# Performance work log

Hardware: AMD Instinct MI355X
Metric: run time of the kernel (lower is better)

Reference implementation:

```python
import jax, jax.numpy as jnp
import numpy as np

N_NODES = 50000
N_EDGES = 500000
N_GRAPHS = 256
D_IN, D_H1, D_H2, D_H3, D_OUT = 768, 256, 128, 64, 2


def _glorot(key, shape):
    fan_in, fan_out = shape[1], shape[0]
    lim = float(np.sqrt(6.0 / (fan_in + fan_out)))
    return jax.random.uniform(key, shape, jnp.float32, -lim, lim)


def setup_inputs() -> dict:
    key = jax.random.key(0)
    ks = jax.random.split(key, 12)
    x = jax.random.normal(ks[0], (N_NODES, D_IN), jnp.float32)
    edge_index = jax.random.randint(ks[1], (2, N_EDGES), 0, N_NODES, jnp.int64)
    batch = jnp.sort(jax.random.randint(ks[2], (N_NODES,), 0, N_GRAPHS, jnp.int64))
    return {
        "x": x,
        "edge_index": edge_index,
        "batch": batch,
        # SAGEConv1: out = lin_l(mean_aggr) + lin_r(x); bias only on lin_l (PyG default)
        "W1_l": _glorot(ks[3], (D_H1, D_IN)),
        "b1_l": jnp.zeros((D_H1,), jnp.float32),
        "W1_r": _glorot(ks[4], (D_H1, D_IN)),
        # SAGEConv2
        "W2_l": _glorot(ks[5], (D_H2, D_H1)),
        "b2_l": jnp.zeros((D_H2,), jnp.float32),
        "W2_r": _glorot(ks[6], (D_H2, D_H1)),
        # MLP head
        "W3": _glorot(ks[7], (D_H3, D_H2)),
        "b3": jnp.zeros((D_H3,), jnp.float32),
        "W4": _glorot(ks[8], (D_OUT, D_H3)),
        "b4": jnp.zeros((D_OUT,), jnp.float32),
    }


def _sage_conv(x, src, dst, deg_inv, W_l, b_l, W_r):
    # mean aggregation of neighbor features: scatter-add then divide by in-degree
    aggr = jax.ops.segment_sum(x[src], dst, num_segments=N_NODES)  # [N, d]
    aggr = aggr * deg_inv[:, None]
    return aggr @ W_l.T + b_l + x @ W_r.T


def reference(x, edge_index, batch, W1_l, b1_l, W1_r, W2_l, b2_l, W2_r, W3, b3, W4, b4):
    src, dst = edge_index[0], edge_index[1]
    deg = jax.ops.segment_sum(jnp.ones((N_EDGES,), x.dtype), dst, num_segments=N_NODES)
    deg_inv = jnp.where(deg > 0, 1.0 / jnp.maximum(deg, 1.0), 0.0)

    h = jax.nn.relu(_sage_conv(x, src, dst, deg_inv, W1_l, b1_l, W1_r))
    h = jax.nn.relu(_sage_conv(h, src, dst, deg_inv, W2_l, b2_l, W2_r))

    # global_mean_pool over graph ids
    pooled = jax.ops.segment_sum(h, batch, num_segments=N_GRAPHS)  # [G, 128]
    cnt = jax.ops.segment_sum(jnp.ones((N_NODES,), h.dtype), batch, num_segments=N_GRAPHS)
    pooled = pooled / jnp.maximum(cnt, 1.0)[:, None]

    # dropout is identity in eval mode
    h = pooled @ W3.T + b3
    h = h @ W4.T + b4
    return jax.nn.softmax(h, axis=-1)
```

## Files before the change

### kernel.cpp

```cpp
#include <hip/hip_runtime.h>
#include <cstdint>
#include <cstddef>

#define N_NODES 50000
#define N_EDGES 500000
#define N_GRAPHS 256
#define D_IN 768
#define D_H1 256
#define D_H2 128

typedef __attribute__((ext_vector_type(8))) __bf16 bf16x8;
typedef __attribute__((ext_vector_type(4))) float f32x4;

__device__ __forceinline__ float bf2f(uint32_t u) {
    union { uint32_t i; float f; } v; v.i = u << 16; return v.f;
}
__device__ __forceinline__ uint32_t f2bf(float f) {
    union { float f; uint32_t i; } v; v.f = f;
    uint32_t u = v.i;
    return (u + 0x7FFFu + ((u >> 16) & 1u)) >> 16;
}

__device__ __forceinline__ void pack_chunk(const float* __restrict__ p,
                                           uint16_t* __restrict__ out, int c) {
    float4 u = *(const float4*)p, v = *(const float4*)(p + 4);
    uint4 o;
    o.x = f2bf(u.x) | (f2bf(u.y) << 16);
    o.y = f2bf(u.z) | (f2bf(u.w) << 16);
    o.z = f2bf(v.x) | (f2bf(v.y) << 16);
    o.w = f2bf(v.z) | (f2bf(v.w) << 16);
    *(uint4*)(out + (size_t)c * 8) = o;
}

#define PACKA_BLKS 18750
#define PACKW1_BLKS 192
#define PACKW2_BLKS 32
#define HIST_BLKS 1954
__global__ __launch_bounds__(256) void k_pack_hist(
    const float* __restrict__ x, uint16_t* __restrict__ xp,
    const float* __restrict__ W1l, const float* __restrict__ W1r, uint16_t* __restrict__ W1p,
    const float* __restrict__ W2l, const float* __restrict__ W2r, uint16_t* __restrict__ W2p,
    const int* __restrict__ e_dst, int* __restrict__ deg)
{
    int b = blockIdx.x;
    if (b < PACKA_BLKS) {
        int c = b * 256 + threadIdx.x;
        int l = c & 63, t = c >> 6;
        int kt = t % 24, mt = t / 24;
        int fr = l & 15, fq = l >> 4;
        pack_chunk(x + (size_t)(mt * 16 + fr) * 768 + kt * 32 + fq * 8, xp, c);
    } else if (b < PACKA_BLKS + PACKW1_BLKS) {
        int c = (b - PACKA_BLKS) * 256 + threadIdx.x;
        int l = c & 63, t = c >> 6;
        int kt = t % 24, mt = t / 24;
        int fr = l & 15, fq = l >> 4;
        int row = mt * 16 + fr;
        const float* src = (row < 256) ? (W1l + (size_t)row * 768)
                                       : (W1r + (size_t)(row - 256) * 768);
        pack_chunk(src + kt * 32 + fq * 8, W1p, c);
    } else if (b < PACKA_BLKS + PACKW1_BLKS + PACKW2_BLKS) {
        int c = (b - PACKA_BLKS - PACKW1_BLKS) * 256 + threadIdx.x;
        int l = c & 63, t = c >> 6;
        int kt = t % 8, mt = t / 8;
        int fr = l & 15, fq = l >> 4;
        int row = mt * 16 + fr;
        const float* src = (row < 128) ? (W2l + (size_t)row * 256)
                                       : (W2r + (size_t)(row - 128) * 256);
        pack_chunk(src + kt * 32 + fq * 8, W2p, c);
    } else {
        int e = (b - PACKA_BLKS - PACKW1_BLKS - PACKW2_BLKS) * 256 + threadIdx.x;
        if (e < N_EDGES) atomicAdd(&deg[e_dst[e]], 1);
    }
}

__global__ void k_scan1(const int* __restrict__ deg, int* __restrict__ row_ex,
                        int* __restrict__ bsum, int n) {
    __shared__ int buf[256];
    int t = threadIdx.x, i = blockIdx.x * 256 + t;
    int v = (i < n) ? deg[i] : 0;
    buf[t] = v; __syncthreads();
    for (int off = 1; off < 256; off <<= 1) {
        int u = (t >= off) ? buf[t - off] : 0;
        __syncthreads(); buf[t] += u; __syncthreads();
    }
    if (i < n) row_ex[i] = buf[t] - v;
    if (t == 255) bsum[blockIdx.x] = buf[255];
}
__global__ void k_scan23(const int* __restrict__ deg, const int* __restrict__ bsum,
                         int* __restrict__ row_start, float* __restrict__ deg_inv,
                         int n, int nb) {
    __shared__ int buf[256];
    int t = threadIdx.x;
    int v = (t < nb) ? bsum[t] : 0;
    buf[t] = v; __syncthreads();
    for (int off = 1; off < 256; off <<= 1) {
        int u = (t >= off) ? buf[t - off] : 0;
        __syncthreads(); buf[t] += u; __syncthreads();
    }
    int b = blockIdx.x;
    int boff = buf[b] - ((b < nb) ? bsum[b] : 0);
    int i = b * 256 + t;
    if (i < n) {
        row_start[i] += boff;
        int d = deg[i];
        deg_inv[i] = (d > 0) ? (1.0f / (float)d) : 0.0f;
    }
    if (b == 0 && t == 0) row_start[n] = N_EDGES;
}

#define G1_BLKS 784
__global__ __launch_bounds__(256, 2) void k_gemm1_fill(
    const uint16_t* __restrict__ Ap, const uint16_t* __restrict__ Bp,
    uint16_t* __restrict__ Cl, uint16_t* __restrict__ Cr,
    const int* __restrict__ e_src, const int* __restrict__ e_dst,
    const int* __restrict__ row_start, int* __restrict__ cursor,
    int* __restrict__ csr_src)
{
    if (blockIdx.x >= G1_BLKS) {
        int e = (blockIdx.x - G1_BLKS) * 256 + threadIdx.x;
        if (e < N_EDGES) {
            int d = e_dst[e];
            int pos = row_start[d] + atomicAdd(&cursor[d], 1);
            csr_src[pos] = e_src[e];
        }
        return;
    }
    const int i = blockIdx.x;
    const int pr = (i >> 4) * 8 + (i & 7);
    const int half = (i >> 3) & 1;
    if (pr >= 391) return;
    const int KT = 24, M = N_NODES;
    const int tid = threadIdx.x;
    const int wave = tid >> 6, lane = tid & 63;
    const int fr = lane & 15, fq = lane >> 4;
    const int bm = pr * 128;
    const int wm = (wave >> 1) * 64, wn = (wave & 1) * 128;
    const int mtiles = (M + 15) >> 4;

    const bf16x8* ap[4];
    const bf16x8* bp[8];
    #pragma unroll
    for (int mi = 0; mi < 4; ++mi) {
        int mt = ((bm + wm) >> 4) + mi;
        if (mt > mtiles - 1) mt = mtiles - 1;
        ap[mi] = (const bf16x8*)Ap + (size_t)mt * KT * 64 + lane;
    }
    #pragma unroll
    for (int ni = 0; ni < 8; ++ni) {
        int nt = ((half * 256 + wn) >> 4) + ni;
        bp[ni] = (const bf16x8*)Bp + (size_t)nt * KT * 64 + lane;
    }

    f32x4 acc[4][8] = {};
    bf16x8 a0[4], b0[8], a1[4], b1[8];

    auto lA = [&](int kt, bf16x8* d) {
        #pragma unroll
        for (int mi = 0; mi < 4; ++mi) d[mi] = ap[mi][kt * 64];
    };
    auto lB = [&](int kt, bf16x8* d) {
        #pragma unroll
        for (int ni = 0; ni < 8; ++ni) d[ni] = bp[ni][kt * 64];
    };
    auto step = [&](bf16x8* a, bf16x8* b) {
        #pragma unroll
        for (int mi = 0; mi < 4; ++mi)
            #pragma unroll
            for (int ni = 0; ni < 8; ++ni)
                acc[mi][ni] = __builtin_amdgcn_mfma_f32_16x16x32_bf16(
                    a[mi], b[ni], acc[mi][ni], 0, 0, 0);
    };

    lA(0, a0); lB(0, b0);
    for (int ks = 0; ks < KT; ks += 2) {
        lA(ks + 1, a1); lB(ks + 1, b1);
        step(a0, b0);
        if (ks + 2 < KT) { lA(ks + 2, a0); lB(ks + 2, b0); }
        step(a1, b1);
    }

    uint16_t* __restrict__ C = half ? Cr : Cl;
    #pragma unroll
    for (int mi = 0; mi < 4; ++mi) {
        #pragma unroll
        for (int r = 0; r < 4; ++r) {
            int row = bm + wm + mi * 16 + fq * 4 + r;
            if (row >= M) continue;
            #pragma unroll
            for (int ni = 0; ni < 8; ++ni) {
                int col = wn + ni * 16 + fr;
                C[(size_t)row * 256 + col] = (uint16_t)f2bf(acc[mi][ni][r]);
            }
        }
    }
}

__global__ __launch_bounds__(256, 2) void k_mgemm(
    const uint16_t* __restrict__ Ap, const uint16_t* __restrict__ Bp,
    uint16_t* __restrict__ C, int M, int N, int KT)
{
    const int tid = threadIdx.x;
    const int wave = tid >> 6, lane = tid & 63;
    const int fr = lane & 15, fq = lane >> 4;
    const int bn = blockIdx.x * 256, bm = blockIdx.y * 128;
    const int wm = (wave >> 1) * 64, wn = (wave & 1) * 128;
    const int mtiles = (M + 15) >> 4;

    const bf16x8* ap[4];
    const bf16x8* bp[8];
    #pragma unroll
    for (int mi = 0; mi < 4; ++mi) {
        int mt = ((bm + wm) >> 4) + mi;
        if (mt > mtiles - 1) mt = mtiles - 1;
        ap[mi] = (const bf16x8*)Ap + (size_t)mt * KT * 64 + lane;
    }
    #pragma unroll
    for (int ni = 0; ni < 8; ++ni) {
        int nt = ((bn + wn) >> 4) + ni;
        bp[ni] = (const bf16x8*)Bp + (size_t)nt * KT * 64 + lane;
    }

    f32x4 acc[4][8] = {};
    bf16x8 a0[4], b0[8], a1[4], b1[8];

    auto lA = [&](int kt, bf16x8* d) {
        #pragma unroll
        for (int mi = 0; mi < 4; ++mi) d[mi] = ap[mi][kt * 64];
    };
    auto lB = [&](int kt, bf16x8* d) {
        #pragma unroll
        for (int ni = 0; ni < 8; ++ni) d[ni] = bp[ni][kt * 64];
    };
    auto step = [&](bf16x8* a, bf16x8* b) {
        #pragma unroll
        for (int mi = 0; mi < 4; ++mi)
            #pragma unroll
            for (int ni = 0; ni < 8; ++ni)
                acc[mi][ni] = __builtin_amdgcn_mfma_f32_16x16x32_bf16(
                    a[mi], b[ni], acc[mi][ni], 0, 0, 0);
    };

    lA(0, a0); lB(0, b0);
    for (int ks = 0; ks < KT; ks += 2) {
        lA(ks + 1, a1); lB(ks + 1, b1);
        step(a0, b0);
        if (ks + 2 < KT) { lA(ks + 2, a0); lB(ks + 2, b0); }
        step(a1, b1);
    }

    #pragma unroll
    for (int mi = 0; mi < 4; ++mi) {
        #pragma unroll
        for (int r = 0; r < 4; ++r) {
            int row = bm + wm + mi * 16 + fq * 4 + r;
            if (row >= M) continue;
            #pragma unroll
            for (int ni = 0; ni < 8; ++ni) {
                int col = bn + wn + ni * 16 + fr;
                C[(size_t)row * N + col] = (uint16_t)f2bf(acc[mi][ni][r]);
            }
        }
    }
}

__global__ __launch_bounds__(256) void k_agg1(
    const uint16_t* __restrict__ yl, const uint16_t* __restrict__ yr,
    const int* __restrict__ row_start, const int* __restrict__ csr,
    const float* __restrict__ deg_inv, const float* __restrict__ bias,
    uint16_t* __restrict__ h1p)
{
    int node = blockIdx.x * 8 + (threadIdx.x >> 5);
    if (node >= N_NODES) return;
    int c = threadIdx.x & 31;
    int s = row_start[node], e = row_start[node + 1];
    float a[8] = {};
    int p = s;
    for (; p + 1 < e; p += 2) {
        uint4 t0 = *(const uint4*)(yl + (size_t)csr[p] * 256 + c * 8);
        uint4 t1 = *(const uint4*)(yl + (size_t)csr[p + 1] * 256 + c * 8);
        a[0] += bf2f(t0.x & 0xFFFF) + bf2f(t1.x & 0xFFFF);
        a[1] += bf2f(t0.x >> 16)    + bf2f(t1.x >> 16);
        a[2] += bf2f(t0.y & 0xFFFF) + bf2f(t1.y & 0xFFFF);
        a[3] += bf2f(t0.y >> 16)    + bf2f(t1.y >> 16);
        a[4] += bf2f(t0.z & 0xFFFF) + bf2f(t1.z & 0xFFFF);
        a[5] += bf2f(t0.z >> 16)    + bf2f(t1.z >> 16);
        a[6] += bf2f(t0.w & 0xFFFF) + bf2f(t1.w & 0xFFFF);
        a[7] += bf2f(t0.w >> 16)    + bf2f(t1.w >> 16);
    }
    if (p < e) {
        uint4 t0 = *(const uint4*)(yl + (size_t)csr[p] * 256 + c * 8);
        a[0] += bf2f(t0.x & 0xFFFF); a[1] += bf2f(t0.x >> 16);
        a[2] += bf2f(t0.y & 0xFFFF); a[3] += bf2f(t0.y >> 16);
        a[4] += bf2f(t0.z & 0xFFFF); a[5] += bf2f(t0.z >> 16);
        a[6] += bf2f(t0.w & 0xFFFF); a[7] += bf2f(t0.w >> 16);
    }
    float w = deg_inv[node];
    uint4 tx = *(const uint4*)(yr + (size_t)node * 256 + c * 8);
    float4 b0 = *(const float4*)(bias + c * 8);
    float4 b1 = *(const float4*)(bias + c * 8 + 4);
    float v0 = fmaxf(a[0] * w + bf2f(tx.x & 0xFFFF) + b0.x, 0.f);
    float v1 = fmaxf(a[1] * w + bf2f(tx.x >> 16)    + b0.y, 0.f);
    float v2 = fmaxf(a[2] * w + bf2f(tx.y & 0xFFFF) + b0.z, 0.f);
    float v3 = fmaxf(a[3] * w + bf2f(tx.y >> 16)    + b0.w, 0.f);
    float v4 = fmaxf(a[4] * w + bf2f(tx.z & 0xFFFF) + b1.x, 0.f);
    float v5 = fmaxf(a[5] * w + bf2f(tx.z >> 16)    + b1.y, 0.f);
    float v6 = fmaxf(a[6] * w + bf2f(tx.w & 0xFFFF) + b1.z, 0.f);
    float v7 = fmaxf(a[7] * w + bf2f(tx.w >> 16)    + b1.w, 0.f);
    uint4 o;
    o.x = f2bf(v0) | (f2bf(v1) << 16);
    o.y = f2bf(v2) | (f2bf(v3) << 16);
    o.z = f2bf(v4) | (f2bf(v5) << 16);
    o.w = f2bf(v6) | (f2bf(v7) << 16);
    uint32_t addr = (((node >> 4) * 8 + (c >> 2)) * 64 + (c & 3) * 16 + (node & 15));
    *(uint4*)(h1p + (size_t)addr * 8) = o;
}

__global__ __launch_bounds__(256) void k_agg2(
    const uint16_t* __restrict__ y, const int* __restrict__ row_start,
    const int* __restrict__ csr, const float* __restrict__ deg_inv,
    const float* __restrict__ bias, float* __restrict__ out)
{
    int node = blockIdx.x * 4 + (threadIdx.x >> 6);
    if (node >= N_NODES) return;
    int lane = threadIdx.x & 63;
    int s = row_start[node], e = row_start[node + 1];
    float a0 = 0.f, a1 = 0.f;
    int p = s;
    for (; p + 1 < e; p += 2) {
        uint32_t t0 = *(const uint32_t*)(y + (size_t)csr[p] * 256 + lane * 2);
        uint32_t t1 = *(const uint32_t*)(y + (size_t)csr[p + 1] * 256 + lane * 2);
        a0 += bf2f(t0 & 0xFFFF) + bf2f(t1 & 0xFFFF);
        a1 += bf2f(t0 >> 16)    + bf2f(t1 >> 16);
    }
    if (p < e) {
        uint32_t t0 = *(const uint32_t*)(y + (size_t)csr[p] * 256 + lane * 2);
        a0 += bf2f(t0 & 0xFFFF);
        a1 += bf2f(t0 >> 16);
    }
    float w = deg_inv[node];
    uint32_t tx = *(const uint32_t*)(y + (size_t)node * 256 + 128 + lane * 2);
    float2 b = *(const float2*)(bias + lane * 2);
    float2 o;
    o.x = fmaxf(a0 * w + bf2f(tx & 0xFFFF) + b.x, 0.f);
    o.y = fmaxf(a1 * w + bf2f(tx >> 16)    + b.y, 0.f);
    *(float2*)(out + (size_t)node * 128 + lane * 2) = o;
}

__global__ void k_poolhead(const float* __restrict__ h2, const int* __restrict__ batch,
                           const float* __restrict__ W3, const float* __restrict__ b3,
                           const float* __restrict__ W4, const float* __restrict__ b4,
                           float* __restrict__ out)
{
    int g = blockIdx.x;
    __shared__ int s_lo, s_hi;
    __shared__ float p[128];
    __shared__ float hid[64];
    __shared__ float logit[2];
    int t = threadIdx.x;
    if (t == 0) {
        int lo = 0, hi = N_NODES;
        while (lo < hi) { int m = (lo + hi) >> 1; if (batch[m] < g) lo = m + 1; else hi = m; }
        s_lo = lo;
        int lo2 = lo, hi2 = N_NODES;
        while (lo2 < hi2) { int m = (lo2 + hi2) >> 1; if (batch[m] < g + 1) lo2 = m + 1; else hi2 = m; }
        s_hi = lo2;
    }
    __syncthreads();
    float sum = 0.f;
    for (int i = s_lo; i < s_hi; ++i) sum += h2[(size_t)i * D_H2 + t];
    int cnt = s_hi - s_lo;
    p[t] = sum / (float)(cnt > 0 ? cnt : 1);
    __syncthreads();
    if (t < 64) {
        float s = b3[t];
        #pragma unroll 4
        for (int k = 0; k < 128; ++k) s = fmaf(p[k], W3[t * 128 + k], s);
        hid[t] = s;
    }
    __syncthreads();
    if (t < 2) {
        float l = b4[t];
        for (int k = 0; k < 64; ++k) l = fmaf(hid[k], W4[t * 64 + k], l);
        logit[t] = l;
    }
    __syncthreads();
    if (t == 0) {
        float m = fmaxf(logit[0], logit[1]);
        float e0 = expf(logit[0] - m), e1 = expf(logit[1] - m);
        float inv = 1.0f / (e0 + e1);
        out[g * 2 + 0] = e0 * inv;
        out[g * 2 + 1] = e1 * inv;
    }
}

extern "C" void kernel_launch(void* const* d_in, const int* in_sizes, int n_in,
                              void* d_out, int out_size, void* d_ws, size_t ws_size,
                              hipStream_t stream)
{
    const float* x     = (const float*)d_in[0];
    const int*   ei    = (const int*)d_in[1];
    const int*   batch = (const int*)d_in[2];
    const float* W1l   = (const float*)d_in[3];
    const float* b1l   = (const float*)d_in[4];
    const float* W1r   = (const float*)d_in[5];
    const float* W2l   = (const float*)d_in[6];
    const float* b2l   = (const float*)d_in[7];
    const float* W2r   = (const float*)d_in[8];
    const float* W3    = (const float*)d_in[9];
    const float* b3    = (const float*)d_in[10];
    const float* W4    = (const float*)d_in[11];
    const float* b4    = (const float*)d_in[12];
    float* out = (float*)d_out;

    const int* e_src = ei;
    const int* e_dst = ei + N_EDGES;

    char* ws = (char*)d_ws;
    size_t off = 0;
    auto alloc = [&](size_t bytes) -> void* {
        void* p = ws + off;
        off = (off + bytes + 255) & ~(size_t)255;
        return p;
    };
    int*      deg       = (int*)alloc((size_t)2 * N_NODES * 4);
    int*      cursor    = deg + N_NODES;
    int*      row_start = (int*)alloc((size_t)(N_NODES + 1) * 4);
    int*      csr_src   = (int*)alloc((size_t)N_EDGES * 4);
    float*    deg_inv   = (float*)alloc((size_t)N_NODES * 4);
    int*      bsum      = (int*)alloc(256 * 4);
    uint16_t* W1p       = (uint16_t*)alloc((size_t)512 * 768 * 2);
    uint16_t* W2p       = (uint16_t*)alloc((size_t)256 * 256 * 2);
    uint16_t* xp        = (uint16_t*)alloc((size_t)N_NODES * D_IN * 2);
    uint16_t* y1        = (uint16_t*)alloc((size_t)N_NODES * 512 * 2);
    uint16_t* h1p       = (uint16_t*)alloc((size_t)N_NODES * 256 * 2);

    uint16_t* y1l = y1;
    uint16_t* y1r = y1 + (size_t)N_NODES * 256;
    uint16_t* y2 = xp;
    float*    h2 = (float*)(xp + (size_t)N_NODES * 256);

    hipMemsetAsync(deg, 0, (size_t)2 * N_NODES * 4, stream);

    k_pack_hist<<<PACKA_BLKS + PACKW1_BLKS + PACKW2_BLKS + HIST_BLKS, 256, 0, stream>>>(
        x, xp, W1l, W1r, W1p, W2l, W2r, W2p, e_dst, deg);

    int nscan = (N_NODES + 255) / 256;
    k_scan1<<<nscan, 256, 0, stream>>>(deg, row_start, bsum, N_NODES);
    k_scan23<<<nscan, 256, 0, stream>>>(deg, bsum, row_start, deg_inv, N_NODES, nscan);

    k_gemm1_fill<<<G1_BLKS + HIST_BLKS, 256, 0, stream>>>(
        xp, W1p, y1l, y1r, e_src, e_dst, row_start, cursor, csr_src);
    k_agg1<<<(N_NODES + 7) / 8, 256, 0, stream>>>(y1l, y1r, row_start, csr_src, deg_inv, b1l, h1p);

    dim3 g2(1, (N_NODES + 127) / 128);
    k_mgemm<<<g2, 256, 0, stream>>>(h1p, W2p, y2, N_NODES, 256, 8);
    k_agg2<<<(N_NODES + 3) / 4, 256, 0, stream>>>(y2, row_start, csr_src, deg_inv, b2l, h2);

    k_poolhead<<<N_GRAPHS, 128, 0, stream>>>(h2, batch, W3, b3, W4, b4, out);
}
```

Measured before the change: 486.8 us.

## Drop x pre-pack, convert fp32 in GEMM1; fuse scans; row-major h1

Removes the separate pass that packed x into an MFMA-tiled bf16 layout. GEMM1 now reads fp32 x directly and converts it with v_cvt_pk_bf16_f32, using 512-thread blocks with 64x64 warp tiles. The two scan kernels are merged into one that spins on per-block sums, and it also initialises the cursor so the CSR fill skips a row_start lookup. h1 is written row-major, so the second GEMM reads A row-major. This saves a full read/write of x and one launch, at the cost of uncoalesced fp32 A loads in GEMM1 and an inter-block spin-wait that relies on all scan blocks being co-resident.

```diff
diff --git a/kernel.cpp b/kernel.cpp
--- a/kernel.cpp
+++ b/kernel.cpp
@@ -19,6 +19,11 @@
     union { float f; uint32_t i; } v; v.f = f;
     uint32_t u = v.i;
     return (u + 0x7FFFu + ((u >> 16) & 1u)) >> 16;
+}
+__device__ __forceinline__ uint32_t cvt_pk_bf16(float lo, float hi) {
+    uint32_t r;
+    asm("v_cvt_pk_bf16_f32 %0, %1, %2" : "=v"(r) : "v"(lo), "v"(hi));
+    return r;
 }
 
 __device__ __forceinline__ void pack_chunk(const float* __restrict__ p,
@@ -32,25 +37,17 @@
     *(uint4*)(out + (size_t)c * 8) = o;
 }
 
-#define PACKA_BLKS 18750
 #define PACKW1_BLKS 192
 #define PACKW2_BLKS 32
-#define HIST_BLKS 1954
-__global__ __launch_bounds__(256) void k_pack_hist(
-    const float* __restrict__ x, uint16_t* __restrict__ xp,
+#define HIST256 1954
+__global__ __launch_bounds__(256) void k_packw_hist(
     const float* __restrict__ W1l, const float* __restrict__ W1r, uint16_t* __restrict__ W1p,
     const float* __restrict__ W2l, const float* __restrict__ W2r, uint16_t* __restrict__ W2p,
     const int* __restrict__ e_dst, int* __restrict__ deg)
 {
     int b = blockIdx.x;
-    if (b < PACKA_BLKS) {
+    if (b < PACKW1_BLKS) {
         int c = b * 256 + threadIdx.x;
-        int l = c & 63, t = c >> 6;
-        int kt = t % 24, mt = t / 24;
-        int fr = l & 15, fq = l >> 4;
-        pack_chunk(x + (size_t)(mt * 16 + fr) * 768 + kt * 32 + fq * 8, xp, c);
-    } else if (b < PACKA_BLKS + PACKW1_BLKS) {
-        int c = (b - PACKA_BLKS) * 256 + threadIdx.x;
         int l = c & 63, t = c >> 6;
         int kt = t % 24, mt = t / 24;
         int fr = l & 15, fq = l >> 4;
@@ -58,8 +55,8 @@
         const float* src = (row < 256) ? (W1l + (size_t)row * 768)
                                        : (W1r + (size_t)(row - 256) * 768);
         pack_chunk(src + kt * 32 + fq * 8, W1p, c);
-    } else if (b < PACKA_BLKS + PACKW1_BLKS + PACKW2_BLKS) {
-        int c = (b - PACKA_BLKS - PACKW1_BLKS) * 256 + threadIdx.x;
+    } else if (b < PACKW1_BLKS + PACKW2_BLKS) {
+        int c = (b - PACKW1_BLKS) * 256 + threadIdx.x;
         int l = c & 63, t = c >> 6;
         int kt = t % 8, mt = t / 8;
         int fr = l & 15, fq = l >> 4;
@@ -68,59 +65,58 @@
                                        : (W2r + (size_t)(row - 128) * 256);
         pack_chunk(src + kt * 32 + fq * 8, W2p, c);
     } else {
-        int e = (b - PACKA_BLKS - PACKW1_BLKS - PACKW2_BLKS) * 256 + threadIdx.x;
+        int e = (b - PACKW1_BLKS - PACKW2_BLKS) * 256 + threadIdx.x;
         if (e < N_EDGES) atomicAdd(&deg[e_dst[e]], 1);
     }
 }
 
-__global__ void k_scan1(const int* __restrict__ deg, int* __restrict__ row_ex,
-                        int* __restrict__ bsum, int n) {
+__global__ __launch_bounds__(256) void k_scan(
+    const int* __restrict__ deg, int* __restrict__ row_start, int* __restrict__ cursor,
+    float* __restrict__ deg_inv, int* __restrict__ bsum, int n, int nb)
+{
     __shared__ int buf[256];
-    int t = threadIdx.x, i = blockIdx.x * 256 + t;
+    __shared__ int bbuf[256];
+    int t = threadIdx.x, b = blockIdx.x, i = b * 256 + t;
     int v = (i < n) ? deg[i] : 0;
     buf[t] = v; __syncthreads();
     for (int off = 1; off < 256; off <<= 1) {
         int u = (t >= off) ? buf[t - off] : 0;
         __syncthreads(); buf[t] += u; __syncthreads();
     }
-    if (i < n) row_ex[i] = buf[t] - v;
-    if (t == 255) bsum[blockIdx.x] = buf[255];
-}
-__global__ void k_scan23(const int* __restrict__ deg, const int* __restrict__ bsum,
-                         int* __restrict__ row_start, float* __restrict__ deg_inv,
-                         int n, int nb) {
-    __shared__ int buf[256];
-    int t = threadIdx.x;
-    int v = (t < nb) ? bsum[t] : 0;
-    buf[t] = v; __syncthreads();
+    if (t == 255) atomicExch(&bsum[b], buf[255] + 1);
+    int w = 0;
+    if (t < nb) {
+        do { w = atomicAdd(&bsum[t], 0); } while (w == 0);
+        w -= 1;
+    }
+    bbuf[t] = w; __syncthreads();
     for (int off = 1; off < 256; off <<= 1) {
-        int u = (t >= off) ? buf[t - off] : 0;
-        __syncthreads(); buf[t] += u; __syncthreads();
-    }
-    int b = blockIdx.x;
-    int boff = buf[b] - ((b < nb) ? bsum[b] : 0);
-    int i = b * 256 + t;
+        int u = (t >= off) ? bbuf[t - off] : 0;
+        __syncthreads(); bbuf[t] += u; __syncthreads();
+    }
+    int base = (b > 0) ? bbuf[b - 1] : 0;
     if (i < n) {
-        row_start[i] += boff;
-        int d = deg[i];
-        deg_inv[i] = (d > 0) ? (1.0f / (float)d) : 0.0f;
+        int rs = base + buf[t] - v;
+        row_start[i] = rs;
+        cursor[i] = rs;
+        deg_inv[i] = (v > 0) ? (1.0f / (float)v) : 0.0f;
     }
     if (b == 0 && t == 0) row_start[n] = N_EDGES;
 }
 
 #define G1_BLKS 784
-__global__ __launch_bounds__(256, 2) void k_gemm1_fill(
-    const uint16_t* __restrict__ Ap, const uint16_t* __restrict__ Bp,
+#define FILL_BLKS 977
+__global__ __launch_bounds__(512, 2) void k_gemm1_fill(
+    const float* __restrict__ X, const uint16_t* __restrict__ Bp,
     uint16_t* __restrict__ Cl, uint16_t* __restrict__ Cr,
     const int* __restrict__ e_src, const int* __restrict__ e_dst,
-    const int* __restrict__ row_start, int* __restrict__ cursor,
-    int* __restrict__ csr_src)
+    int* __restrict__ cursor, int* __restrict__ csr_src)
 {
     if (blockIdx.x >= G1_BLKS) {
-        int e = (blockIdx.x - G1_BLKS) * 256 + threadIdx.x;
+        int e = (blockIdx.x - G1_BLKS) * 512 + threadIdx.x;
         if (e < N_EDGES) {
             int d = e_dst[e];
-            int pos = row_start[d] + atomicAdd(&cursor[d], 1);
+            int pos = atomicAdd(&cursor[d], 1);
             csr_src[pos] = e_src[e];
         }
         return;
@@ -129,54 +125,68 @@
     const int pr = (i >> 4) * 8 + (i & 7);
     const int half = (i >> 3) & 1;
     if (pr >= 391) return;
-    const int KT = 24, M = N_NODES;
+    const int KT = 24;
     const int tid = threadIdx.x;
     const int wave = tid >> 6, lane = tid & 63;
     const int fr = lane & 15, fq = lane >> 4;
     const int bm = pr * 128;
-    const int wm = (wave >> 1) * 64, wn = (wave & 1) * 128;
-    const int mtiles = (M + 15) >> 4;
-
-    const bf16x8* ap[4];
-    const bf16x8* bp[8];
+    const int wm = (wave >> 2) * 64, wn = (wave & 3) * 64;
+
+    const float* aptr[4];
     #pragma unroll
     for (int mi = 0; mi < 4; ++mi) {
-        int mt = ((bm + wm) >> 4) + mi;
-        if (mt > mtiles - 1) mt = mtiles - 1;
-        ap[mi] = (const bf16x8*)Ap + (size_t)mt * KT * 64 + lane;
-    }
-    #pragma unroll
-    for (int ni = 0; ni < 8; ++ni) {
+        int rb = bm + wm + mi * 16;
+        if (rb > N_NODES - 16) rb = N_NODES - 16;
+        aptr[mi] = X + (size_t)(rb + fr) * 768 + fq * 8;
+    }
+    const bf16x8* bp[4];
+    #pragma unroll
+    for (int ni = 0; ni < 4; ++ni) {
         int nt = ((half * 256 + wn) >> 4) + ni;
         bp[ni] = (const bf16x8*)Bp + (size_t)nt * KT * 64 + lane;
     }
 
-    f32x4 acc[4][8] = {};
-    bf16x8 a0[4], b0[8], a1[4], b1[8];
-
-    auto lA = [&](int kt, bf16x8* d) {
-        #pragma unroll
-        for (int mi = 0; mi < 4; ++mi) d[mi] = ap[mi][kt * 64];
+    f32x4 acc[4][4] = {};
+    float4 af0[8], af1[8];
+    bf16x8 b0[4], b1[4];
+
+    auto lA = [&](int kt, float4* d) {
+        #pragma unroll
+        for (int mi = 0; mi < 4; ++mi) {
+            const float* p = aptr[mi] + kt * 32;
+            d[mi * 2]     = *(const float4*)p;
+            d[mi * 2 + 1] = *(const float4*)(p + 4);
+        }
     };
     auto lB = [&](int kt, bf16x8* d) {
         #pragma unroll
-        for (int ni = 0; ni < 8; ++ni) d[ni] = bp[ni][kt * 64];
-    };
-    auto step = [&](bf16x8* a, bf16x8* b) {
+        for (int ni = 0; ni < 4; ++ni) d[ni] = bp[ni][kt * 64];
+    };
+    auto step = [&](const float4* af, bf16x8* b) {
+        bf16x8 a[4];
+        #pragma unroll
+        for (int mi = 0; mi < 4; ++mi) {
+            union { bf16x8 v; uint32_t u[4]; } t;
+            t.u[0] = cvt_pk_bf16(af[mi * 2].x,     af[mi * 2].y);
+            t.u[1] = cvt_pk_bf16(af[mi * 2].z,     af[mi * 2].w);
+            t.u[2] = cvt_pk_bf16(af[mi * 2 + 1].x, af[mi * 2 + 1].y);
+            t.u[3] = cvt_pk_bf16(af[mi * 2 + 1].z, af[mi * 2 + 1].w);
+            a[mi] = t.v;
+        }
         #pragma unroll
         for (int mi = 0; mi < 4; ++mi)
             #pragma unroll
-            for (int ni = 0; ni < 8; ++ni)
+            for (int ni = 0; ni < 4; ++ni)
                 acc[mi][ni] = __builtin_amdgcn_mfma_f32_16x16x32_bf16(
                     a[mi], b[ni], acc[mi][ni], 0, 0, 0);
     };
 
-    lA(0, a0); lB(0, b0);
+    lA(0, af0); lB(0, b0);
     for (int ks = 0; ks < KT; ks += 2) {
-        lA(ks + 1, a1); lB(ks + 1, b1);
-        step(a0, b0);
-        if (ks + 2 < KT) { lA(ks + 2, a0); lB(ks + 2, b0); }
-        step(a1, b1);
+        lA(ks + 1, af1); lB(ks + 1, b1);
+        step(af0, b0);
+        if (ks + 2 < KT) { lA(ks + 2, af0); lB(ks + 2, b0); }
+        step(af1, b1);
     }
 
     uint16_t* __restrict__ C = half ? Cr : Cl;
@@ -185,9 +195,9 @@
         #pragma unroll
         for (int r = 0; r < 4; ++r) {
             int row = bm + wm + mi * 16 + fq * 4 + r;
-            if (row >= M) continue;
+            if (row >= N_NODES) continue;
             #pragma unroll
-            for (int ni = 0; ni < 8; ++ni) {
+            for (int ni = 0; ni < 4; ++ni) {
                 int col = wn + ni * 16 + fr;
                 C[(size_t)row * 256 + col] = (uint16_t)f2bf(acc[mi][ni][r]);
             }
@@ -195,25 +205,25 @@
     }
 }
 
-__global__ __launch_bounds__(256, 2) void k_mgemm(
-    const uint16_t* __restrict__ Ap, const uint16_t* __restrict__ Bp,
+__global__ __launch_bounds__(256, 2) void k_mgemm_rm(
+    const uint16_t* __restrict__ A, const uint16_t* __restrict__ Bp,
     uint16_t* __restrict__ C, int M, int N, int KT)
 {
+    const int K = KT * 32;
     const int tid = threadIdx.x;
     const int wave = tid >> 6, lane = tid & 63;
     const int fr = lane & 15, fq = lane >> 4;
     const int bn = blockIdx.x * 256, bm = blockIdx.y * 128;
     const int wm = (wave >> 1) * 64, wn = (wave & 1) * 128;
-    const int mtiles = (M + 15) >> 4;
-
-    const bf16x8* ap[4];
+
+    const uint16_t* ap[4];
+    #pragma unroll
+    for (int mi = 0; mi < 4; ++mi) {
+        int rb = bm + wm + mi * 16;
+        if (rb > M - 16) rb = M - 16;
+        ap[mi] = A + (size_t)(rb + fr) * K + fq * 8;
+    }
     const bf16x8* bp[8];
-    #pragma unroll
-    for (int mi = 0; mi < 4; ++mi) {
-        int mt = ((bm + wm) >> 4) + mi;
-        if (mt > mtiles - 1) mt = mtiles - 1;
-        ap[mi] = (const bf16x8*)Ap + (size_t)mt * KT * 64 + lane;
-    }
     #pragma unroll
     for (int ni = 0; ni < 8; ++ni) {
         int nt = ((bn + wn) >> 4) + ni;
@@ -225,7 +235,7 @@
 
     auto lA = [&](int kt, bf16x8* d) {
         #pragma unroll
-        for (int mi = 0; mi < 4; ++mi) d[mi] = ap[mi][kt * 64];
+        for (int mi = 0; mi < 4; ++mi) d[mi] = *(const bf16x8*)(ap[mi] + kt * 32);
     };
     auto lB = [&](int kt, bf16x8* d) {
         #pragma unroll
@@ -267,7 +277,7 @@
     const uint16_t* __restrict__ yl, const uint16_t* __restrict__ yr,
     const int* __restrict__ row_start, const int* __restrict__ csr,
     const float* __restrict__ deg_inv, const float* __restrict__ bias,
-    uint16_t* __restrict__ h1p)
+    uint16_t* __restrict__ h1)
 {
     int node = blockIdx.x * 8 + (threadIdx.x >> 5);
     if (node >= N_NODES) return;
@@ -311,8 +321,7 @@
     o.y = f2bf(v2) | (f2bf(v3) << 16);
     o.z = f2bf(v4) | (f2bf(v5) << 16);
     o.w = f2bf(v6) | (f2bf(v7) << 16);
-    uint32_t addr = (((node >> 4) * 8 + (c >> 2)) * 64 + (c & 3) * 16 + (node & 15));
-    *(uint4*)(h1p + (size_t)addr * 8) = o;
+    *(uint4*)(h1 + (size_t)node * 256 + c * 8) = o;
 }
 
 __global__ __launch_bounds__(256) void k_agg2(
@@ -422,38 +431,36 @@
         off = (off + bytes + 255) & ~(size_t)255;
         return p;
     };
-    int*      deg       = (int*)alloc((size_t)2 * N_NODES * 4);
-    int*      cursor    = deg + N_NODES;
+    int*      deg       = (int*)alloc((size_t)(N_NODES + 256) * 4);
+    int*      bsum      = deg + N_NODES;
     int*      row_start = (int*)alloc((size_t)(N_NODES + 1) * 4);
+    int*      cursor    = (int*)alloc((size_t)N_NODES * 4);
     int*      csr_src   = (int*)alloc((size_t)N_EDGES * 4);
     float*    deg_inv   = (float*)alloc((size_t)N_NODES * 4);
-    int*      bsum      = (int*)alloc(256 * 4);
     uint16_t* W1p       = (uint16_t*)alloc((size_t)512 * 768 * 2);
     uint16_t* W2p       = (uint16_t*)alloc((size_t)256 * 256 * 2);
-    uint16_t* xp        = (uint16_t*)alloc((size_t)N_NODES * D_IN * 2);
     uint16_t* y1        = (uint16_t*)alloc((size_t)N_NODES * 512 * 2);
-    uint16_t* h1p       = (uint16_t*)alloc((size_t)N_NODES * 256 * 2);
+    uint16_t* h1        = (uint16_t*)alloc((size_t)N_NODES * 256 * 2);
+    uint16_t* y2        = (uint16_t*)alloc((size_t)N_NODES * 256 * 2);
+    float*    h2        = (float*)alloc((size_t)N_NODES * 128 * 4);
 
     uint16_t* y1l = y1;
     uint16_t* y1r = y1 + (size_t)N_NODES * 256;
-    uint16_t* y2 = xp;
-    float*    h2 = (float*)(xp + (size_t)N_NODES * 256);
-
-    hipMemsetAsync(deg, 0, (size_t)2 * N_NODES * 4, stream);
-
-    k_pack_hist<<<PACKA_BLKS + PACKW1_BLKS + PACKW2_BLKS + HIST_BLKS, 256, 0, stream>>>(
-        x, xp, W1l, W1r, W1p, W2l, W2r, W2p, e_dst, deg);
+
+    hipMemsetAsync(deg, 0, (size_t)(N_NODES + 256) * 4, stream);
+
+    k_packw_hist<<<PACKW1_BLKS + PACKW2_BLKS + HIST256, 256, 0, stream>>>(
+        W1l, W1r, W1p, W2l, W2r, W2p, e_dst, deg);
 
     int nscan = (N_NODES + 255) / 256;
-    k_scan1<<<nscan, 256, 0, stream>>>(deg, row_start, bsum, N_NODES);
-    k_scan23<<<nscan, 256, 0, stream>>>(deg, bsum, row_start, deg_inv, N_NODES, nscan);
-
-    k_gemm1_fill<<<G1_BLKS + HIST_BLKS, 256, 0, stream>>>(
-        xp, W1p, y1l, y1r, e_src, e_dst, row_start, cursor, csr_src);
-    k_agg1<<<(N_NODES + 7) / 8, 256, 0, stream>>>(y1l, y1r, row_start, csr_src, deg_inv, b1l, h1p);
+    k_scan<<<nscan, 256, 0, stream>>>(deg, row_start, cursor, deg_inv, bsum, N_NODES, nscan);
+
+    k_gemm1_fill<<<G1_BLKS + FILL_BLKS, 512, 0, stream>>>(
+        x, W1p, y1l, y1r, e_src, e_dst, cursor, csr_src);
+    k_agg1<<<(N_NODES + 7) / 8, 256, 0, stream>>>(y1l, y1r, row_start, csr_src, deg_inv, b1l, h1);
 
     dim3 g2(1, (N_NODES + 127) / 128);
-    k_mgemm<<<g2, 256, 0, stream>>>(h1p, W2p, y2, N_NODES, 256, 8);
+    k_mgemm_rm<<<g2, 256, 0, stream>>>(h1, W2p, y2, N_NODES, 256, 8);
     k_agg2<<<(N_NODES + 3) / 4, 256, 0, stream>>>(y2, row_start, csr_src, deg_inv, b2l, h2);
 
     k_poolhead<<<N_GRAPHS, 128, 0, stream>>>(h2, batch, W3, b3, W4, b4, out);
```

New measurement: 601.7 us. 1.24x slower.
